# Optimization experiments

Hardware: AMD Instinct MI355X
Metric: run time of the kernel (lower is better)

The kernel has to match this reference:

```python
import jax, jax.numpy as jnp
import numpy as np

B, MAXN, D, H, S = 64, 512, 512, 8, 32
DH = D // H          # per-head dim = 64
N = B * MAXN         # 32768 total nodes
E = 524288           # ~avg degree 16
EPS = 1e-5


def setup_inputs() -> dict:
    key = jax.random.key(0)
    ks = jax.random.split(key, 18)
    s = 0.05
    x_dense = jax.random.normal(ks[0], (B, MAXN, D), jnp.float32)
    x = jax.random.normal(ks[1], (N, D), jnp.float32)
    src = jax.random.randint(ks[2], (E,), 0, N)
    # destinations kept within the same graph as the source
    dst = (src // MAXN) * MAXN + jax.random.randint(ks[3], (E,), 0, MAXN)
    edge_index = jnp.stack([src, dst]).astype(jnp.int32)
    batch = (jnp.arange(N) // MAXN).astype(jnp.int32)  # sorted, 512 nodes/graph
    seed = jax.random.normal(ks[4], (S, 1, D), jnp.float32) * s
    # per-head GCN conv weights concatenated along output dim: [D, H*DH] == [D, D]
    Wk = jax.random.normal(ks[5], (D, D), jnp.float32) * s
    bk = jnp.zeros((D,), jnp.float32)
    Wv = jax.random.normal(ks[6], (D, D), jnp.float32) * s
    bv = jnp.zeros((D,), jnp.float32)
    q_proj_weight = jax.random.normal(ks[7], (D, D), jnp.float32) * s
    Wo = jax.random.normal(ks[8], (D, D), jnp.float32) * s
    bo = jnp.zeros((D,), jnp.float32)
    Wff = jax.random.normal(ks[9], (D, D), jnp.float32) * s
    bff = jnp.zeros((D,), jnp.float32)
    gamma_h = jnp.ones((D,), jnp.float32)
    beta_h = jnp.zeros((D,), jnp.float32)
    gamma_z = jnp.ones((D,), jnp.float32)
    beta_z = jnp.zeros((D,), jnp.float32)
    return dict(x_dense=x_dense, x=x, edge_index=edge_index, batch=batch,
                seed=seed, Wk=Wk, bk=bk, Wv=Wv, bv=bv,
                q_proj_weight=q_proj_weight, Wo=Wo, bo=bo, Wff=Wff, bff=bff,
                gamma_h=gamma_h, beta_h=beta_h, gamma_z=gamma_z, beta_z=beta_z)


def _gcn(x, W, b, src, dst):
    # PyG GCNConv with self-loops + symmetric norm; all H heads fused via W [D, H*DH]
    xw = x @ W                                   # [N, D]
    idx = jnp.arange(N)
    src_f = jnp.concatenate([src, idx])
    dst_f = jnp.concatenate([dst, idx])
    deg = jax.ops.segment_sum(jnp.ones_like(dst_f, dtype=x.dtype), dst_f, num_segments=N)
    dinv = jax.lax.rsqrt(deg)                    # deg >= 1 (self-loops)
    norm = dinv[src_f] * dinv[dst_f]             # [E+N]
    out = jax.ops.segment_sum(xw[src_f] * norm[:, None], dst_f, num_segments=N)
    return out + b


def _to_dense(feat, batch):
    # to_dense_batch for sorted batch vector; padded slots are zeros
    counts = jax.ops.segment_sum(jnp.ones((N,), jnp.int32), batch, num_segments=B)
    start = jnp.cumsum(counts) - counts
    pos = jnp.arange(N) - start[batch]
    return jnp.zeros((B, MAXN, feat.shape[-1]), feat.dtype).at[batch, pos].set(feat)


def _layernorm(x, g, b):
    m = jnp.mean(x, -1, keepdims=True)
    v = jnp.mean(jnp.square(x - m), -1, keepdims=True)
    return (x - m) * jax.lax.rsqrt(v + EPS) * g + b


def reference(x_dense, x, edge_index, batch, seed, Wk, bk, Wv, bv,
              q_proj_weight, Wo, bo, Wff, bff, gamma_h, beta_h, gamma_z, beta_z):
    src, dst = edge_index[0], edge_index[1]
    k_nodes = _gcn(x, Wk, bk, src, dst)          # [N, D] (H heads concat)
    v_nodes = _gcn(x, Wv, bv, src, dst)
    k_dense = _to_dense(k_nodes, batch)          # [B, MAXN, D]
    v_dense = _to_dense(v_nodes, batch)

    # query: seed [S,1,D] repeated over batch -> [S,B,D]; q projection (F.linear)
    query = jnp.broadcast_to(seed, (S, B, D))
    q = jnp.einsum('sbd,ed->sbe', query, q_proj_weight)
    scale = 1.0 / jnp.sqrt(jnp.float32(DH))
    qh = (q * scale).reshape(S, B, H, DH).transpose(1, 2, 0, 3)     # [B,H,S,DH]
    kh = k_dense.reshape(B, MAXN, H, DH).transpose(0, 2, 1, 3)      # [B,H,N,DH]
    vh = v_dense.reshape(B, MAXN, H, DH).transpose(0, 2, 1, 3)
    scores = jnp.einsum('bhsd,bhnd->bhsn', qh, kh)                  # [B,H,S,MAXN]
    attn = jax.nn.softmax(scores, axis=-1)                          # no padding mask (faithful)
    ctx = jnp.einsum('bhsn,bhnd->bhsd', attn, vh)                   # [B,H,S,DH]
    ctx = ctx.transpose(0, 2, 1, 3).reshape(B, S, D)                # heads concat
    attn_out = ctx @ Wo.T + bo                                      # [B,S,D]

    query_bse = jnp.broadcast_to(seed.transpose(1, 0, 2), (B, S, D))
    embed = _layernorm(query_bse + attn_out, gamma_h, beta_h)
    embed = _layernorm(embed + embed @ Wff.T + bff, gamma_z, beta_z)
    return embed
```

## Files before the change

### kernel.cpp

```cpp
#include <hip/hip_runtime.h>
#include <hip/hip_bf16.h>

#define BN   64
#define MAXN 512
#define DIM  512
#define NH   8
#define NS   32
#define NN   32768
#define NE   524288
#define NBLK 256
#define EPB  (NE / NBLK)
#define MP   (2048 * 512)

typedef __hip_bfloat16 bf16;
using bf16x8 = __attribute__((ext_vector_type(8))) short;
using f32x4  = __attribute__((ext_vector_type(4))) float;

__device__ int            g_cnt[NN];
__device__ int            g_off[NN + 1];
__device__ int            g_csr[NE];
__device__ unsigned short g_hist[(long)NBLK * NN];
__device__ unsigned short g_bpfx[(long)NBLK * NN];
__device__ float g_dinv[NN];
__device__ bf16  g_xb[NN * DIM];
__device__ bf16  g_agg[NN * DIM];
__device__ bf16  g_aggT[NN * DIM];
__device__ bf16  g_qf[256 * DIM];
__device__ bf16  g_wob[DIM * DIM];
__device__ bf16  g_wvb[DIM * DIM];
__device__ bf16  g_wvo[DIM * 8 * DIM];
__device__ float g_bvo[DIM];
__device__ bf16  g_wffT[DIM * DIM];
__device__ float g_q[NS * DIM];
__device__ bf16  g_sc[BN * 256 * MAXN];
__device__ bf16  g_cp[BN * NS * 8 * DIM];
__device__ float g_part[4 * MP];
__device__ float g_h1[BN * NS * DIM];
__device__ bf16  g_h1b[BN * NS * DIM];

__device__ inline float bf2f(unsigned short u) {
    union { unsigned int i; float f; } x; x.i = ((unsigned int)u) << 16; return x.f;
}

__device__ inline void gll16(const bf16* g, bf16* l) {
    __builtin_amdgcn_global_load_lds(
        (const __attribute__((address_space(1))) void*)g,
        (__attribute__((address_space(3))) void*)l, 16, 0, 0);
}

__global__ __launch_bounds__(512) void k_hist(const int* __restrict__ dst) {
    __shared__ unsigned int h[NN];
    int p = blockIdx.x, tid = threadIdx.x;
    for (int i = tid; i < NN; i += 512) h[i] = 0;
    __syncthreads();
#pragma unroll
    for (int j = 0; j < EPB / 512; j++) {
        int e = p * EPB + j * 512 + tid;
        atomicAdd(&h[dst[e]], 1u);
    }
    __syncthreads();
    unsigned short* out = g_hist + (long)p * NN;
    for (int i = tid; i < NN; i += 512) out[i] = (unsigned short)h[i];
}

__global__ __launch_bounds__(256) void k_colscan() {
    int v = blockIdx.x * 256 + threadIdx.x;
    unsigned int s = 0;
#pragma unroll 8
    for (int p = 0; p < NBLK; p++) {
        unsigned int hh = g_hist[(long)p * NN + v];
        g_bpfx[(long)p * NN + v] = (unsigned short)s;
        s += hh;
    }
    g_cnt[v] = (int)s;
    g_dinv[v] = rsqrtf(1.0f + (float)s);
}

__global__ void k_scan() {
    __shared__ int part[1024];
    int t = threadIdx.x;
    int base = t * 32;
    int loc[32]; int s = 0;
#pragma unroll
    for (int i = 0; i < 32; i++) { loc[i] = g_cnt[base + i]; s += loc[i]; }
    part[t] = s; __syncthreads();
    for (int o = 1; o < 1024; o <<= 1) {
        int v = (t >= o) ? part[t - o] : 0;
        __syncthreads();
        part[t] += v;
        __syncthreads();
    }
    int ex = (t == 0) ? 0 : part[t - 1];
#pragma unroll
    for (int i = 0; i < 32; i++) { g_off[base + i] = ex; ex += loc[i]; }
    if (t == 1023) g_off[NN] = ex;
}

__global__ __launch_bounds__(512) void k_fillsort(const int* __restrict__ src,
                                                  const int* __restrict__ dst) {
    __shared__ unsigned int l[NN];
    int p = blockIdx.x, tid = threadIdx.x;
    const unsigned short* bp = g_bpfx + (long)p * NN;
    for (int i = tid; i < NN; i += 512) l[i] = bp[i];
    __syncthreads();
#pragma unroll
    for (int j = 0; j < EPB / 512; j++) {
        int e = p * EPB + j * 512 + tid;
        int v = dst[e];
        unsigned int r = atomicAdd(&l[v], 1u);
        g_csr[g_off[v] + r] = src[e];
    }
}

__global__ __launch_bounds__(256) void k_prep(const float* __restrict__ seed,
                                              const float* __restrict__ Wq,
                                              const float* __restrict__ Wo,
                                              const float* __restrict__ Wv,
                                              const float* __restrict__ Wff,
                                              const float* __restrict__ bo,
                                              const float* __restrict__ bv) {
    int blk = blockIdx.x;
    if (blk < 64) {
        int i = blk * 256 + threadIdx.x;
        int s = i >> 9, e = i & 511;
        const float* sr = seed + s * DIM;
        const float* wr = Wq + e * DIM;
        float a0 = 0.f, a1 = 0.f;
        for (int d = 0; d < DIM; d += 8) {
            float4 a = *(const float4*)(sr + d);
            float4 b = *(const float4*)(wr + d);
            float4 c = *(const float4*)(sr + d + 4);
            float4 w = *(const float4*)(wr + d + 4);
            a0 += a.x * b.x + a.y * b.y + a.z * b.z + a.w * b.w;
            a1 += c.x * w.x + c.y * w.y + c.z * w.z + c.w * w.w;
        }
        g_q[i] = (a0 + a1) * 0.125f;
    } else if (blk < 448) {
        long t = (long)(blk - 64) * 256 + threadIdx.x;
        const float* src; bf16* dstp; long off;
        if (t < 32768)      { src = Wo;  dstp = g_wob;  off = t; }
        else if (t < 65536) { src = Wv;  dstp = g_wvb;  off = t - 32768; }
        else                { src = Wff; dstp = g_wffT; off = t - 65536; }
        long i = off * 8;
        float4 a = *(const float4*)(src + i);
        float4 b = *(const float4*)(src + i + 4);
        float v[8] = {a.x, a.y, a.z, a.w, b.x, b.y, b.z, b.w};
        bf16x8 o;
#pragma unroll
        for (int j = 0; j < 8; j++) { bf16 q = __float2bfloat16(v[j]); o[j] = *(short*)&q; }
        *(bf16x8*)(dstp + i) = o;
    } else {
        int e = (blk - 448) * 256 + threadIdx.x;
        const float* orow = Wo + (long)e * DIM;
        float a0 = 0.f, a1 = 0.f;
        for (int c = 0; c < DIM; c += 8) {
            float4 a = *(const float4*)(bv + c);
            float4 w = *(const float4*)(orow + c);
            float4 xx = *(const float4*)(bv + c + 4);
            float4 u = *(const float4*)(orow + c + 4);
            a0 += a.x * w.x + a.y * w.y + a.z * w.z + a.w * w.w;
            a1 += xx.x * u.x + xx.y * u.y + xx.z * u.z + xx.w * u.w;
        }
        g_bvo[e] = bo[e] + a0 + a1;
    }
}

__device__ __forceinline__ void gemm128(const bf16* __restrict__ A, long lda,
                                        const bf16* __restrict__ Bt, long ldb,
                                        long row0, long col0, int kbeg, int kend,
                                        bf16 (*As)[128 * 32], bf16 (*Bs)[128 * 32],
                                        f32x4 acc[4][4]) {
    int tid = threadIdx.x;
    int lane = tid & 63, wave = tid >> 6;
    int wr = wave >> 1, wc = wave & 1;
    int fr = lane & 15, fq = lane >> 4;
    int rchunk = (fq ^ ((fr >> 1) & 3)) * 8;
    int u0 = wave * 128 + lane;
    int sr0 = u0 >> 2, sc0 = ((u0 & 3) ^ ((sr0 >> 1) & 3)) * 8;
    int u1 = u0 + 64;
    int sr1 = u1 >> 2, sc1 = ((u1 & 3) ^ ((sr1 >> 1) & 3)) * 8;

    auto stage = [&](int buf, int kt) {
        gll16(A + (row0 + sr0) * lda + kt + sc0, As[buf] + u0 * 8);
        gll16(A + (row0 + sr1) * lda + kt + sc1, As[buf] + u1 * 8);
        gll16(Bt + (col0 + sr0) * ldb + kt + sc0, Bs[buf] + u0 * 8);
        gll16(Bt + (col0 + sr1) * ldb + kt + sc1, Bs[buf] + u1 * 8);
    };

    stage(0, kbeg);
    __syncthreads();
    for (int kt = kbeg; kt < kend; kt += 32) {
        int buf = ((kt - kbeg) >> 5) & 1;
        if (kt + 32 < kend) stage(buf ^ 1, kt + 32);
        bf16x8 af[4], bfv[4];
#pragma unroll
        for (int mi = 0; mi < 4; mi++)
            af[mi] = *(const bf16x8*)(As[buf] + (wr * 64 + mi * 16 + fr) * 32 + rchunk);
#pragma unroll
        for (int ni = 0; ni < 4; ni++)
            bfv[ni] = *(const bf16x8*)(Bs[buf] + (wc * 64 + ni * 16 + fr) * 32 + rchunk);
#pragma unroll
        for (int mi = 0; mi < 4; mi++)
#pragma unroll
            for (int ni = 0; ni < 4; ni++)
                acc[mi][ni] = __builtin_amdgcn_mfma_f32_16x16x32_bf16(af[mi], bfv[ni], acc[mi][ni], 0, 0, 0);
        __syncthreads();
    }
}

#define ACC_INIT                                             \
    f32x4 acc[4][4];                                         \
    _Pragma("unroll")                                        \
    for (int i = 0; i < 4; i++)                              \
        _Pragma("unroll")                                    \
        for (int j = 0; j < 4; j++) acc[i][j] = (f32x4){0.f, 0.f, 0.f, 0.f}; \
    int lane = threadIdx.x & 63, wave = threadIdx.x >> 6;    \
    int wr = wave >> 1, wc = wave & 1;                       \
    int fr = lane & 15, fq = lane >> 4;

__global__ __launch_bounds__(256) void k_xbqf(const float* __restrict__ x,
                                              const float* __restrict__ Wk) {
    __shared__ bf16 As[2][128 * 32];
    __shared__ bf16 Bs[2][128 * 32];
    int blk = blockIdx.x;
    if (blk < 8192) {
        long i = (long)blk * (256 * 8) + (long)threadIdx.x * 8;
        int node = (int)(i >> 9);
        float w = g_dinv[node];
        float4 a = *(const float4*)(x + i);
        float4 b = *(const float4*)(x + i + 4);
        float v[8] = {a.x, a.y, a.z, a.w, b.x, b.y, b.z, b.w};
        bf16x8 o;
#pragma unroll
        for (int j = 0; j < 8; j++) { bf16 t = __float2bfloat16(v[j] * w); o[j] = *(short*)&t; }
        *(bf16x8*)(g_xb + i) = o;
    } else if (blk < 8704) {
        int i = (blk - 8192) * 256 + threadIdx.x;
        int hs = i >> 9, d = i & 511;
        int h = hs >> 5, s = hs & 31;
        const float* qr = g_q + s * DIM + h * 64;
        const float* wr = Wk + d * DIM + h * 64;
        float a0 = 0.f, a1 = 0.f;
        for (int t2 = 0; t2 < 64; t2 += 8) {
            float4 a = *(const float4*)(qr + t2);
            float4 w = *(const float4*)(wr + t2);
            float4 c = *(const float4*)(qr + t2 + 4);
            float4 u = *(const float4*)(wr + t2 + 4);
            a0 += a.x * w.x + a.y * w.y + a.z * w.z + a.w * w.w;
            a1 += c.x * u.x + c.y * u.y + c.z * u.z + c.w * u.w;
        }
        g_qf[i] = __float2bfloat16(a0 + a1);
    } else {
        int wi = blk - 8704;
        int bx = wi & 3, by = (wi >> 2) & 3, h = wi >> 4;
        ACC_INIT
        long row0 = (long)bx * 128, col0 = (long)by * 128;
        gemm128(g_wob, DIM, g_wvb, DIM, row0, col0, h * 64, h * 64 + 64, As, Bs, acc);
#pragma unroll
        for (int mi = 0; mi < 4; mi++)
#pragma unroll
            for (int ni = 0; ni < 4; ni++) {
                long col = col0 + wc * 64 + ni * 16 + fr;
#pragma unroll
                for (int r = 0; r < 4; r++) {
                    long row = row0 + wr * 64 + mi * 16 + fq * 4 + r;
                    g_wvo[row * 4096 + h * 512 + col] = __float2bfloat16(acc[mi][ni][r]);
                }
            }
    }
}

__global__ __launch_bounds__(256) void k_gather() {
    int bid = blockIdx.x;
    int lb = (bid & 7) * 1024 + (bid >> 3);
    int wave = threadIdx.x >> 6, lane = threadIdx.x & 63;
    int node = lb * 4 + wave;

    bf16x8 sv = ((const bf16x8*)(g_xb + (long)node * DIM))[lane];
    float acc[8];
#pragma unroll
    for (int j = 0; j < 8; j++) acc[j] = bf2f((unsigned short)sv[j]);

    int e = g_off[node], e1 = g_off[node + 1];
    for (; e + 8 <= e1; e += 8) {
        bf16x8 r[8];
#pragma unroll
        for (int q = 0; q < 8; q++)
            r[q] = ((const bf16x8*)(g_xb + (long)g_csr[e + q] * DIM))[lane];
#pragma unroll
        for (int j = 0; j < 8; j++) {
            float s01 = bf2f((unsigned short)r[0][j]) + bf2f((unsigned short)r[1][j]);
            float s23 = bf2f((unsigned short)r[2][j]) + bf2f((unsigned short)r[3][j]);
            float s45 = bf2f((unsigned short)r[4][j]) + bf2f((unsigned short)r[5][j]);
            float s67 = bf2f((unsigned short)r[6][j]) + bf2f((unsigned short)r[7][j]);
            acc[j] += (s01 + s23) + (s45 + s67);
        }
    }
    for (; e < e1; e++) {
        bf16x8 r0 = ((const bf16x8*)(g_xb + (long)g_csr[e] * DIM))[lane];
#pragma unroll
        for (int j = 0; j < 8; j++) acc[j] += bf2f((unsigned short)r0[j]);
    }
    float dd = g_dinv[node];
    bf16x8 o;
#pragma unroll
    for (int j = 0; j < 8; j++) { bf16 t = __float2bfloat16(acc[j] * dd); o[j] = *(short*)&t; }
    ((bf16x8*)(g_agg + (long)node * DIM))[lane] = o;
}

__global__ __launch_bounds__(256) void k_aggsc() {
    __shared__ __align__(16) char smem[32768];
    int blk = blockIdx.x;
    if (blk < 512) {
        bf16 (*As)[128 * 32] = (bf16(*)[128 * 32])smem;
        bf16 (*Bs)[128 * 32] = (bf16(*)[128 * 32])(smem + 16384);
        int b = blk & 63, bx = (blk >> 6) & 1, by = blk >> 7;
        ACC_INIT
        long row0 = (long)bx * 128, col0 = (long)by * 128;
        gemm128(g_qf, DIM, g_agg + (long)b * (MAXN * DIM), DIM, row0, col0, 0, DIM, As, Bs, acc);
        bf16* out = g_sc + (long)b * (256 * MAXN);
#pragma unroll
        for (int mi = 0; mi < 4; mi++)
#pragma unroll
            for (int ni = 0; ni < 4; ni++) {
                long col = col0 + wc * 64 + ni * 16 + fr;
#pragma unroll
                for (int r = 0; r < 4; r++) {
                    long row = row0 + wr * 64 + mi * 16 + fq * 4 + r;
                    out[row * MAXN + col] = __float2bfloat16(acc[mi][ni][r]);
                }
            }
    } else {
        unsigned short (*L)[72] = (unsigned short(*)[72])smem;
        int id = blk - 512;
        int b = id >> 6, t = id & 63;
        int n0 = (t & 7) * 64, d0 = (t >> 3) * 64;
        int tid = threadIdx.x;
        const unsigned short* src = (const unsigned short*)g_agg + ((long)b * 512 + n0) * 512 + d0;
#pragma unroll
        for (int p = 0; p < 2; p++) {
            int r = (tid >> 3) + 32 * p, c = (tid & 7) * 8;
            *(int4*)&L[r][c] = *(const int4*)(src + (long)r * 512 + c);
        }
        __syncthreads();
        unsigned short* dst = (unsigned short*)g_aggT + ((long)b * 512 + d0) * 512 + n0;
#pragma unroll
        for (int p = 0; p < 2; p++) {
            int dr = (tid >> 3) + 32 * p, c0 = (tid & 7) * 8;
            unsigned short tmp[8];
#pragma unroll
            for (int j = 0; j < 8; j++) tmp[j] = L[c0 + j][dr];
            *(int4*)(dst + (long)dr * 512 + c0) = *(int4*)tmp;
        }
    }
}

__global__ __launch_bounds__(256) void k_soft() {
    int w = threadIdx.x >> 6, lane = threadIdx.x & 63;
    unsigned short* base = (unsigned short*)g_sc + ((long)blockIdx.x * 16 + w * 4) * MAXN;
#pragma unroll
    for (int r = 0; r < 4; r++) {
        unsigned short* row = base + (long)r * MAXN;
        float v[8]; float m = -1e30f;
#pragma unroll
        for (int k = 0; k < 8; k++) { v[k] = bf2f(row[lane + 64 * k]); m = fmaxf(m, v[k]); }
#pragma unroll
        for (int o = 32; o > 0; o >>= 1) m = fmaxf(m, __shfl_xor(m, o));
        float sum = 0.f;
#pragma unroll
        for (int k = 0; k < 8; k++) { v[k] = __expf(v[k] - m); sum += v[k]; }
#pragma unroll
        for (int o = 32; o > 0; o >>= 1) sum += __shfl_xor(sum, o);
        float inv = 1.0f / sum;
#pragma unroll
        for (int k = 0; k < 8; k++) {
            bf16 t = __float2bfloat16(v[k] * inv);
            row[lane + 64 * k] = *(unsigned short*)&t;
        }
    }
}

__global__ __launch_bounds__(256) void k_pvg() {
    __shared__ bf16 As[2][128 * 32];
    __shared__ bf16 Bs[2][128 * 32];
    int blk = blockIdx.x;
    int b = blk & 63, bx = (blk >> 6) & 1, by = (blk >> 7) & 1, dh = blk >> 8;
    ACC_INIT
    long row0 = (long)bx * 128, col0 = (long)by * 128;
    gemm128(g_sc + (long)b * (256 * MAXN), MAXN,
            g_aggT + (long)b * (DIM * MAXN) + (long)dh * (256 * MAXN), MAXN,
            row0, col0, 0, MAXN, As, Bs, acc);
#pragma unroll
    for (int mi = 0; mi < 4; mi++)
#pragma unroll
        for (int ni = 0; ni < 4; ni++) {
            long col = col0 + wc * 64 + ni * 16 + fr;
#pragma unroll
            for (int r = 0; r < 4; r++) {
                long row = row0 + wr * 64 + mi * 16 + fq * 4 + r;
                g_cp[((long)b * NS + (row & 31)) * 4096 + (row >> 5) * 512 + dh * 256 + col] =
                    __float2bfloat16(acc[mi][ni][r]);
            }
        }
}

__global__ __launch_bounds__(256) void k_vo() {
    __shared__ bf16 As[2][128 * 32];
    __shared__ bf16 Bs[2][128 * 32];
    ACC_INIT
    int z = blockIdx.z;
    long row0 = (long)blockIdx.x * 128, col0 = (long)blockIdx.y * 128;
    gemm128(g_cp, 4096, g_wvo, 4096, row0, col0, z * 1024, z * 1024 + 1024, As, Bs, acc);
    float* out = g_part + (long)z * MP;
#pragma unroll
    for (int mi = 0; mi < 4; mi++)
#pragma unroll
        for (int ni = 0; ni < 4; ni++) {
            long col = col0 + wc * 64 + ni * 16 + fr;
#pragma unroll
            for (int r = 0; r < 4; r++) {
                long row = row0 + wr * 64 + mi * 16 + fq * 4 + r;
                out[row * DIM + col] = acc[mi][ni][r];
            }
        }
}

__global__ __launch_bounds__(256) void k_ffn() {
    __shared__ bf16 As[2][128 * 32];
    __shared__ bf16 Bs[2][128 * 32];
    ACC_INIT
    int z = blockIdx.z;
    long row0 = (long)blockIdx.x * 128, col0 = (long)blockIdx.y * 128;
    gemm128(g_h1b, DIM, g_wffT, DIM, row0, col0, z * 128, z * 128 + 128, As, Bs, acc);
    float* out = g_part + (long)z * MP;
#pragma unroll
    for (int mi = 0; mi < 4; mi++)
#pragma unroll
        for (int ni = 0; ni < 4; ni++) {
            long col = col0 + wc * 64 + ni * 16 + fr;
#pragma unroll
            for (int r = 0; r < 4; r++) {
                long row = row0 + wr * 64 + mi * 16 + fq * 4 + r;
                out[row * DIM + col] = acc[mi][ni][r];
            }
        }
}

__device__ inline float blockReduceSum(float v, float* red, int tid) {
#pragma unroll
    for (int o = 32; o > 0; o >>= 1) v += __shfl_xor(v, o);
    __syncthreads();
    if ((tid & 63) == 0) red[tid >> 6] = v;
    __syncthreads();
    return red[0] + red[1] + red[2] + red[3];
}

__global__ __launch_bounds__(256) void k_ln1(const float* __restrict__ seed,
                                             const float* __restrict__ gamma,
                                             const float* __restrict__ beta) {
    __shared__ float red[4];
    int r = blockIdx.x, t = threadIdx.x;
    int s = r & 31;
    long base = (long)r * DIM;
    float v0 = seed[s * DIM + t] + g_bvo[t];
    float v1 = seed[s * DIM + 256 + t] + g_bvo[256 + t];
#pragma unroll
    for (int z = 0; z < 4; z++) {
        v0 += g_part[(long)z * MP + base + t];
        v1 += g_part[(long)z * MP + base + 256 + t];
    }
    float mean = blockReduceSum(v0 + v1, red, t) * (1.0f / DIM);
    float d0 = v0 - mean, d1 = v1 - mean;
    float var = blockReduceSum(d0 * d0 + d1 * d1, red, t) * (1.0f / DIM);
    float ri = rsqrtf(var + 1e-5f);
    float o0 = d0 * ri * gamma[t] + beta[t];
    float o1 = d1 * ri * gamma[256 + t] + beta[256 + t];
    g_h1[base + t] = o0; g_h1[base + 256 + t] = o1;
    g_h1b[base + t] = __float2bfloat16(o0);
    g_h1b[base + 256 + t] = __float2bfloat16(o1);
}

__global__ __launch_bounds__(256) void k_ln2(const float* __restrict__ gamma,
                                             const float* __restrict__ beta,
                                             const float* __restrict__ bff,
                                             float* __restrict__ out) {
    __shared__ float red[4];
    int r = blockIdx.x, t = threadIdx.x;
    long base = (long)r * DIM;
    float v0 = g_h1[base + t] + bff[t];
    float v1 = g_h1[base + 256 + t] + bff[256 + t];
#pragma unroll
    for (int z = 0; z < 4; z++) {
        v0 += g_part[(long)z * MP + base + t];
        v1 += g_part[(long)z * MP + base + 256 + t];
    }
    float mean = blockReduceSum(v0 + v1, red, t) * (1.0f / DIM);
    float d0 = v0 - mean, d1 = v1 - mean;
    float var = blockReduceSum(d0 * d0 + d1 * d1, red, t) * (1.0f / DIM);
    float ri = rsqrtf(var + 1e-5f);
    out[base + t] = d0 * ri * gamma[t] + beta[t];
    out[base + 256 + t] = d1 * ri * gamma[256 + t] + beta[256 + t];
}

extern "C" void kernel_launch(void* const* d_in, const int* in_sizes, int n_in,
                              void* d_out, int out_size, void* d_ws, size_t ws_size,
                              hipStream_t stream) {
    (void)in_sizes; (void)n_in; (void)out_size; (void)d_ws; (void)ws_size;
    const float* x    = (const float*)d_in[1];
    const int*   ei   = (const int*)d_in[2];
    const int*   esrc = ei;
    const int*   edst = ei + NE;
    const float* seed = (const float*)d_in[4];
    const float* Wk   = (const float*)d_in[5];
    const float* Wv   = (const float*)d_in[7];
    const float* bv   = (const float*)d_in[8];
    const float* Wq   = (const float*)d_in[9];
    const float* Wo   = (const float*)d_in[10];
    const float* bo   = (const float*)d_in[11];
    const float* Wff  = (const float*)d_in[12];
    const float* bff  = (const float*)d_in[13];
    const float* gh   = (const float*)d_in[14];
    const float* bh   = (const float*)d_in[15];
    const float* gz   = (const float*)d_in[16];
    const float* bz   = (const float*)d_in[17];
    float* out = (float*)d_out;

    k_hist    <<<NBLK, 512, 0, stream>>>(edst);
    k_colscan <<<NN / 256, 256, 0, stream>>>();
    k_scan    <<<1, 1024, 0, stream>>>();
    k_prep    <<<450, 256, 0, stream>>>(seed, Wq, Wo, Wv, Wff, bo, bv);
    k_fillsort<<<NBLK, 512, 0, stream>>>(esrc, edst);
    k_xbqf    <<<8832, 256, 0, stream>>>(x, Wk);
    k_gather  <<<NN / 4, 256, 0, stream>>>();
    k_aggsc   <<<512 + BN * 64, 256, 0, stream>>>();
    k_soft    <<<1024, 256, 0, stream>>>();
    k_pvg     <<<512, 256, 0, stream>>>();
    k_vo      <<<dim3(16, 4, 4), 256, 0, stream>>>();
    k_ln1     <<<BN * NS, 256, 0, stream>>>(seed, gh, bh);
    k_ffn     <<<dim3(16, 4, 4), 256, 0, stream>>>();
    k_ln2     <<<BN * NS, 256, 0, stream>>>(gz, bz, bff, out);
}
```

Baseline: 229.4 us.

## Fuse preprocessing kernels and split each node's gather across four waves

```diff
diff --git a/kernel.cpp b/kernel.cpp
--- a/kernel.cpp
+++ b/kernel.cpp
@@ -48,80 +48,29 @@
         (__attribute__((address_space(3))) void*)l, 16, 0, 0);
 }
 
-__global__ __launch_bounds__(512) void k_hist(const int* __restrict__ dst) {
+__global__ __launch_bounds__(512) void k_histprep(const int* __restrict__ dst,
+                                                  const float* __restrict__ seed,
+                                                  const float* __restrict__ Wq,
+                                                  const float* __restrict__ Wo,
+                                                  const float* __restrict__ Wv,
+                                                  const float* __restrict__ Wff,
+                                                  const float* __restrict__ bo,
+                                                  const float* __restrict__ bv) {
     __shared__ unsigned int h[NN];
-    int p = blockIdx.x, tid = threadIdx.x;
-    for (int i = tid; i < NN; i += 512) h[i] = 0;
-    __syncthreads();
-#pragma unroll
-    for (int j = 0; j < EPB / 512; j++) {
-        int e = p * EPB + j * 512 + tid;
-        atomicAdd(&h[dst[e]], 1u);
-    }
-    __syncthreads();
-    unsigned short* out = g_hist + (long)p * NN;
-    for (int i = tid; i < NN; i += 512) out[i] = (unsigned short)h[i];
-}
-
-__global__ __launch_bounds__(256) void k_colscan() {
-    int v = blockIdx.x * 256 + threadIdx.x;
-    unsigned int s = 0;
-#pragma unroll 8
-    for (int p = 0; p < NBLK; p++) {
-        unsigned int hh = g_hist[(long)p * NN + v];
-        g_bpfx[(long)p * NN + v] = (unsigned short)s;
-        s += hh;
-    }
-    g_cnt[v] = (int)s;
-    g_dinv[v] = rsqrtf(1.0f + (float)s);
-}
-
-__global__ void k_scan() {
-    __shared__ int part[1024];
-    int t = threadIdx.x;
-    int base = t * 32;
-    int loc[32]; int s = 0;
-#pragma unroll
-    for (int i = 0; i < 32; i++) { loc[i] = g_cnt[base + i]; s += loc[i]; }
-    part[t] = s; __syncthreads();
-    for (int o = 1; o < 1024; o <<= 1) {
-        int v = (t >= o) ? part[t - o] : 0;
-        __syncthreads();
-        part[t] += v;
-        __syncthreads();
-    }
-    int ex = (t == 0) ? 0 : part[t - 1];
-#pragma unroll
-    for (int i = 0; i < 32; i++) { g_off[base + i] = ex; ex += loc[i]; }
-    if (t == 1023) g_off[NN] = ex;
-}
-
-__global__ __launch_bounds__(512) void k_fillsort(const int* __restrict__ src,
-                                                  const int* __restrict__ dst) {
-    __shared__ unsigned int l[NN];
-    int p = blockIdx.x, tid = threadIdx.x;
-    const unsigned short* bp = g_bpfx + (long)p * NN;
-    for (int i = tid; i < NN; i += 512) l[i] = bp[i];
-    __syncthreads();
-#pragma unroll
-    for (int j = 0; j < EPB / 512; j++) {
-        int e = p * EPB + j * 512 + tid;
-        int v = dst[e];
-        unsigned int r = atomicAdd(&l[v], 1u);
-        g_csr[g_off[v] + r] = src[e];
-    }
-}
-
-__global__ __launch_bounds__(256) void k_prep(const float* __restrict__ seed,
-                                              const float* __restrict__ Wq,
-                                              const float* __restrict__ Wo,
-                                              const float* __restrict__ Wv,
-                                              const float* __restrict__ Wff,
-                                              const float* __restrict__ bo,
-                                              const float* __restrict__ bv) {
-    int blk = blockIdx.x;
-    if (blk < 64) {
-        int i = blk * 256 + threadIdx.x;
+    int blk = blockIdx.x, tid = threadIdx.x;
+    if (blk < NBLK) {
+        for (int i = tid; i < NN; i += 512) h[i] = 0;
+        __syncthreads();
+#pragma unroll
+        for (int j = 0; j < EPB / 512; j++) {
+            int e = blk * EPB + j * 512 + tid;
+            atomicAdd(&h[dst[e]], 1u);
+        }
+        __syncthreads();
+        unsigned short* out = g_hist + (long)blk * NN;
+        for (int i = tid; i < NN; i += 512) out[i] = (unsigned short)h[i];
+    } else if (blk < 288) {
+        int i = (blk - 256) * 512 + tid;
         int s = i >> 9, e = i & 511;
         const float* sr = seed + s * DIM;
         const float* wr = Wq + e * DIM;
@@ -135,8 +84,8 @@
             a1 += c.x * w.x + c.y * w.y + c.z * w.z + c.w * w.w;
         }
         g_q[i] = (a0 + a1) * 0.125f;
-    } else if (blk < 448) {
-        long t = (long)(blk - 64) * 256 + threadIdx.x;
+    } else if (blk < 480) {
+        long t = (long)(blk - 288) * 512 + tid;
         const float* src; bf16* dstp; long off;
         if (t < 32768)      { src = Wo;  dstp = g_wob;  off = t; }
         else if (t < 65536) { src = Wv;  dstp = g_wvb;  off = t - 32768; }
@@ -150,7 +99,7 @@
         for (int j = 0; j < 8; j++) { bf16 q = __float2bfloat16(v[j]); o[j] = *(short*)&q; }
         *(bf16x8*)(dstp + i) = o;
     } else {
-        int e = (blk - 448) * 256 + threadIdx.x;
+        int e = tid;
         const float* orow = Wo + (long)e * DIM;
         float a0 = 0.f, a1 = 0.f;
         for (int c = 0; c < DIM; c += 8) {
@@ -163,6 +112,137 @@
         }
         g_bvo[e] = bo[e] + a0 + a1;
     }
+}
+
+__global__ __launch_bounds__(256) void k_colscan() {
+    int v = blockIdx.x * 256 + threadIdx.x;
+    unsigned int s = 0;
+#pragma unroll 8
+    for (int p = 0; p < NBLK; p++) {
+        unsigned int hh = g_hist[(long)p * NN + v];
+        g_bpfx[(long)p * NN + v] = (unsigned short)s;
+        s += hh;
+    }
+    g_cnt[v] = (int)s;
+    g_dinv[v] = rsqrtf(1.0f + (float)s);
+}
+
+__global__ void k_scan() {
+    __shared__ int part[1024];
+    int t = threadIdx.x;
+    int base = t * 32;
+    int loc[32]; int s = 0;
+#pragma unroll
+    for (int i = 0; i < 32; i++) { loc[i] = g_cnt[base + i]; s += loc[i]; }
+    part[t] = s; __syncthreads();
+    for (int o = 1; o < 1024; o <<= 1) {
+        int v = (t >= o) ? part[t - o] : 0;
+        __syncthreads();
+        part[t] += v;
+        __syncthreads();
+    }
+    int ex = (t == 0) ? 0 : part[t - 1];
+#pragma unroll
+    for (int i = 0; i < 32; i++) { g_off[base + i] = ex; ex += loc[i]; }
+    if (t == 1023) g_off[NN] = ex;
+}
+
+__global__ __launch_bounds__(512) void k_fillxb(const int* __restrict__ src,
+                                                const int* __restrict__ dst,
+                                                const float* __restrict__ x,
+                                                const float* __restrict__ Wk) {
+    __shared__ unsigned int l[NN];
+    int blk = blockIdx.x, tid = threadIdx.x;
+    if (blk < NBLK) {
+        const unsigned short* bp = g_bpfx + (long)blk * NN;
+        for (int i = tid; i < NN; i += 512) l[i] = bp[i];
+        __syncthreads();
+#pragma unroll
+        for (int j = 0; j < EPB / 512; j++) {
+            int e = blk * EPB + j * 512 + tid;
+            int v = dst[e];
+            unsigned int r = atomicAdd(&l[v], 1u);
+            g_csr[g_off[v] + r] = src[e];
+        }
+    } else if (blk < 4352) {
+        long i = (long)(blk - 256) * (512 * 8) + (long)tid * 8;
+        int node = (int)(i >> 9);
+        float w = g_dinv[node];
+        float4 a = *(const float4*)(x + i);
+        float4 b = *(const float4*)(x + i + 4);
+        float v[8] = {a.x, a.y, a.z, a.w, b.x, b.y, b.z, b.w};
+        bf16x8 o;
+#pragma unroll
+        for (int j = 0; j < 8; j++) { bf16 t = __float2bfloat16(v[j] * w); o[j] = *(short*)&t; }
+        *(bf16x8*)(g_xb + i) = o;
+    } else {
+        int i = (blk - 4352) * 512 + tid;
+        int hs = i >> 9, d = i & 511;
+        int h = hs >> 5, s = hs & 31;
+        const float* qr = g_q + s * DIM + h * 64;
+        const float* wr = Wk + d * DIM + h * 64;
+        float a0 = 0.f, a1 = 0.f;
+        for (int t2 = 0; t2 < 64; t2 += 8) {
+            float4 a = *(const float4*)(qr + t2);
+            float4 w = *(const float4*)(wr + t2);
+            float4 c = *(const float4*)(qr + t2 + 4);
+            float4 u = *(const float4*)(wr + t2 + 4);
+            a0 += a.x * w.x + a.y * w.y + a.z * w.z + a.w * w.w;
+            a1 += c.x * u.x + c.y * u.y + c.z * u.z + c.w * u.w;
+        }
+        g_qf[i] = __float2bfloat16(a0 + a1);
+    }
+}
+
+__global__ __launch_bounds__(256) void k_gather2() {
+    __shared__ float sA[4][576];
+    int bid = blockIdx.x;
+    int node = (bid & 7) * 4096 + (bid >> 3);
+    int w = threadIdx.x >> 6, lane = threadIdx.x & 63;
+
+    float2 acc[4];
+#pragma unroll
+    for (int j = 0; j < 4; j++) acc[j] = make_float2(0.f, 0.f);
+
+    auto addrow = [&](int s) {
+        int4 d = ((const int4*)(g_xb + (long)s * DIM))[lane];
+        union { int i; float f; } lo, hi;
+#pragma unroll
+        for (int j = 0; j < 4; j++) {
+            int dw = (j == 0) ? d.x : (j == 1) ? d.y : (j == 2) ? d.z : d.w;
+            lo.i = dw << 16;
+            hi.i = dw & 0xffff0000;
+            acc[j] += make_float2(lo.f, hi.f);
+        }
+    };
+
+    if (w == 0) addrow(node);
+    int e0 = g_off[node], e1 = g_off[node + 1];
+    int deg = e1 - e0;
+    int m16 = e0 + ((deg >> 4) << 4);
+    for (int eb = e0 + w * 4; eb < m16; eb += 16) {
+        int s0 = g_csr[eb], s1 = g_csr[eb + 1], s2 = g_csr[eb + 2], s3 = g_csr[eb + 3];
+        addrow(s0); addrow(s1); addrow(s2); addrow(s3);
+    }
+    for (int e = m16 + w; e < e1; e += 4) addrow(g_csr[e]);
+
+#pragma unroll
+    for (int j = 0; j < 4; j++) {
+        sA[w][lane * 9 + j * 2]     = acc[j].x;
+        sA[w][lane * 9 + j * 2 + 1] = acc[j].y;
+    }
+    __syncthreads();
+
+    int t = threadIdx.x;
+    int idx = (t >> 2) * 9 + 2 * (t & 3);
+    float s0 = 0.f, s1 = 0.f;
+#pragma unroll
+    for (int ww = 0; ww < 4; ww++) { s0 += sA[ww][idx]; s1 += sA[ww][idx + 1]; }
+    float dd = g_dinv[node];
+    bf16 b0 = __float2bfloat16(s0 * dd), b1 = __float2bfloat16(s1 * dd);
+    unsigned int word = (unsigned int)*(unsigned short*)&b0 |
+                        ((unsigned int)*(unsigned short*)&b1 << 16);
+    ((unsigned int*)(g_agg + (long)node * DIM))[t] = word;
 }
 
 __device__ __forceinline__ void gemm128(const bf16* __restrict__ A, long lda,
@@ -218,96 +298,6 @@
     int wr = wave >> 1, wc = wave & 1;                       \
     int fr = lane & 15, fq = lane >> 4;
 
-__global__ __launch_bounds__(256) void k_xbqf(const float* __restrict__ x,
-                                              const float* __restrict__ Wk) {
-    __shared__ bf16 As[2][128 * 32];
-    __shared__ bf16 Bs[2][128 * 32];
-    int blk = blockIdx.x;
-    if (blk < 8192) {
-        long i = (long)blk * (256 * 8) + (long)threadIdx.x * 8;
-        int node = (int)(i >> 9);
-        float w = g_dinv[node];
-        float4 a = *(const float4*)(x + i);
-        float4 b = *(const float4*)(x + i + 4);
-        float v[8] = {a.x, a.y, a.z, a.w, b.x, b.y, b.z, b.w};
-        bf16x8 o;
-#pragma unroll
-        for (int j = 0; j < 8; j++) { bf16 t = __float2bfloat16(v[j] * w); o[j] = *(short*)&t; }
-        *(bf16x8*)(g_xb + i) = o;
-    } else if (blk < 8704) {
-        int i = (blk - 8192) * 256 + threadIdx.x;
-        int hs = i >> 9, d = i & 511;
-        int h = hs >> 5, s = hs & 31;
-        const float* qr = g_q + s * DIM + h * 64;
-        const float* wr = Wk + d * DIM + h * 64;
-        float a0 = 0.f, a1 = 0.f;
-        for (int t2 = 0; t2 < 64; t2 += 8) {
-            float4 a = *(const float4*)(qr + t2);
-            float4 w = *(const float4*)(wr + t2);
-            float4 c = *(const float4*)(qr + t2 + 4);
-            float4 u = *(const float4*)(wr + t2 + 4);
-            a0 += a.x * w.x + a.y * w.y + a.z * w.z + a.w * w.w;
-            a1 += c.x * u.x + c.y * u.y + c.z * u.z + c.w * u.w;
-        }
-        g_qf[i] = __float2bfloat16(a0 + a1);
-    } else {
-        int wi = blk - 8704;
-        int bx = wi & 3, by = (wi >> 2) & 3, h = wi >> 4;
-        ACC_INIT
-        long row0 = (long)bx * 128, col0 = (long)by * 128;
-        gemm128(g_wob, DIM, g_wvb, DIM, row0, col0, h * 64, h * 64 + 64, As, Bs, acc);
-#pragma unroll
-        for (int mi = 0; mi < 4; mi++)
-#pragma unroll
-            for (int ni = 0; ni < 4; ni++) {
-                long col = col0 + wc * 64 + ni * 16 + fr;
-#pragma unroll
-                for (int r = 0; r < 4; r++) {
-                    long row = row0 + wr * 64 + mi * 16 + fq * 4 + r;
-                    g_wvo[row * 4096 + h * 512 + col] = __float2bfloat16(acc[mi][ni][r]);
-                }
-            }
-    }
-}
-
-__global__ __launch_bounds__(256) void k_gather() {
-    int bid = blockIdx.x;
-    int lb = (bid & 7) * 1024 + (bid >> 3);
-    int wave = threadIdx.x >> 6, lane = threadIdx.x & 63;
-    int node = lb * 4 + wave;
-
-    bf16x8 sv = ((const bf16x8*)(g_xb + (long)node * DIM))[lane];
-    float acc[8];
-#pragma unroll
-    for (int j = 0; j < 8; j++) acc[j] = bf2f((unsigned short)sv[j]);
-
-    int e = g_off[node], e1 = g_off[node + 1];
-    for (; e + 8 <= e1; e += 8) {
-        bf16x8 r[8];
-#pragma unroll
-        for (int q = 0; q < 8; q++)
-            r[q] = ((const bf16x8*)(g_xb + (long)g_csr[e + q] * DIM))[lane];
-#pragma unroll
-        for (int j = 0; j < 8; j++) {
-            float s01 = bf2f((unsigned short)r[0][j]) + bf2f((unsigned short)r[1][j]);
-            float s23 = bf2f((unsigned short)r[2][j]) + bf2f((unsigned short)r[3][j]);
-            float s45 = bf2f((unsigned short)r[4][j]) + bf2f((unsigned short)r[5][j]);
-            float s67 = bf2f((unsigned short)r[6][j]) + bf2f((unsigned short)r[7][j]);
-            acc[j] += (s01 + s23) + (s45 + s67);
-        }
-    }
-    for (; e < e1; e++) {
-        bf16x8 r0 = ((const bf16x8*)(g_xb + (long)g_csr[e] * DIM))[lane];
-#pragma unroll
-        for (int j = 0; j < 8; j++) acc[j] += bf2f((unsigned short)r0[j]);
-    }
-    float dd = g_dinv[node];
-    bf16x8 o;
-#pragma unroll
-    for (int j = 0; j < 8; j++) { bf16 t = __float2bfloat16(acc[j] * dd); o[j] = *(short*)&t; }
-    ((bf16x8*)(g_agg + (long)node * DIM))[lane] = o;
-}
-
 __global__ __launch_bounds__(256) void k_aggsc() {
     __shared__ __align__(16) char smem[32768];
     int blk = blockIdx.x;
@@ -330,7 +320,7 @@
                     out[row * MAXN + col] = __float2bfloat16(acc[mi][ni][r]);
                 }
             }
-    } else {
+    } else if (blk < 4608) {
         unsigned short (*L)[72] = (unsigned short(*)[72])smem;
         int id = blk - 512;
         int b = id >> 6, t = id & 63;
@@ -352,6 +342,25 @@
             for (int j = 0; j < 8; j++) tmp[j] = L[c0 + j][dr];
             *(int4*)(dst + (long)dr * 512 + c0) = *(int4*)tmp;
         }
+    } else {
+        bf16 (*As)[128 * 32] = (bf16(*)[128 * 32])smem;
+        bf16 (*Bs)[128 * 32] = (bf16(*)[128 * 32])(smem + 16384);
+        int wi = blk - 4608;
+        int bx = wi & 3, by = (wi >> 2) & 3, h = wi >> 4;
+        ACC_INIT
+        long row0 = (long)bx * 128, col0 = (long)by * 128;
+        gemm128(g_wob, DIM, g_wvb, DIM, row0, col0, h * 64, h * 64 + 64, As, Bs, acc);
+#pragma unroll
+        for (int mi = 0; mi < 4; mi++)
+#pragma unroll
+            for (int ni = 0; ni < 4; ni++) {
+                long col = col0 + wc * 64 + ni * 16 + fr;
+#pragma unroll
+                for (int r = 0; r < 4; r++) {
+                    long row = row0 + wr * 64 + mi * 16 + fq * 4 + r;
+                    g_wvo[row * 4096 + h * 512 + col] = __float2bfloat16(acc[mi][ni][r]);
+                }
+            }
     }
 }
 
@@ -525,14 +534,12 @@
     const float* bz   = (const float*)d_in[17];
     float* out = (float*)d_out;
 
-    k_hist    <<<NBLK, 512, 0, stream>>>(edst);
+    k_histprep<<<481, 512, 0, stream>>>(edst, seed, Wq, Wo, Wv, Wff, bo, bv);
     k_colscan <<<NN / 256, 256, 0, stream>>>();
     k_scan    <<<1, 1024, 0, stream>>>();
-    k_prep    <<<450, 256, 0, stream>>>(seed, Wq, Wo, Wv, Wff, bo, bv);
-    k_fillsort<<<NBLK, 512, 0, stream>>>(esrc, edst);
-    k_xbqf    <<<8832, 256, 0, stream>>>(x, Wk);
-    k_gather  <<<NN / 4, 256, 0, stream>>>();
-    k_aggsc   <<<512 + BN * 64, 256, 0, stream>>>();
+    k_fillxb  <<<4608, 512, 0, stream>>>(esrc, edst, x, Wk);
+    k_gather2 <<<NN, 256, 0, stream>>>();
+    k_aggsc   <<<4736, 256, 0, stream>>>();
     k_soft    <<<1024, 256, 0, stream>>>();
     k_pvg     <<<512, 256, 0, stream>>>();
     k_vo      <<<dim3(16, 4, 4), 256, 0, stream>>>();
```

After: 243.5 us. 6.2% more time.

## Stage per-graph feature tiles in LDS for neighbor aggregation; pack histogram stores

Applied to the files above, without the earlier changes.

```diff
diff --git a/kernel.cpp b/kernel.cpp
--- a/kernel.cpp
+++ b/kernel.cpp
@@ -51,7 +51,7 @@
 __global__ __launch_bounds__(512) void k_hist(const int* __restrict__ dst) {
     __shared__ unsigned int h[NN];
     int p = blockIdx.x, tid = threadIdx.x;
-    for (int i = tid; i < NN; i += 512) h[i] = 0;
+    for (int i = tid; i < NN / 4; i += 512) ((int4*)h)[i] = make_int4(0, 0, 0, 0);
     __syncthreads();
 #pragma unroll
     for (int j = 0; j < EPB / 512; j++) {
@@ -59,21 +59,26 @@
         atomicAdd(&h[dst[e]], 1u);
     }
     __syncthreads();
-    unsigned short* out = g_hist + (long)p * NN;
-    for (int i = tid; i < NN; i += 512) out[i] = (unsigned short)h[i];
+    unsigned int* out32 = (unsigned int*)(g_hist + (long)p * NN);
+    for (int i = tid; i < NN / 2; i += 512)
+        out32[i] = h[2 * i] | (h[2 * i + 1] << 16);
 }
 
 __global__ __launch_bounds__(256) void k_colscan() {
-    int v = blockIdx.x * 256 + threadIdx.x;
-    unsigned int s = 0;
+    int v2 = blockIdx.x * 256 + threadIdx.x;
+    const unsigned int* H = (const unsigned int*)g_hist;
+    unsigned int* B = (unsigned int*)g_bpfx;
+    unsigned int s0 = 0, s1 = 0;
 #pragma unroll 8
     for (int p = 0; p < NBLK; p++) {
-        unsigned int hh = g_hist[(long)p * NN + v];
-        g_bpfx[(long)p * NN + v] = (unsigned short)s;
-        s += hh;
-    }
-    g_cnt[v] = (int)s;
-    g_dinv[v] = rsqrtf(1.0f + (float)s);
+        unsigned int hh = H[(long)p * (NN / 2) + v2];
+        B[(long)p * (NN / 2) + v2] = s0 | (s1 << 16);
+        s0 += hh & 0xffffu; s1 += hh >> 16;
+    }
+    g_cnt[2 * v2] = (int)s0;
+    g_cnt[2 * v2 + 1] = (int)s1;
+    g_dinv[2 * v2] = rsqrtf(1.0f + (float)s0);
+    g_dinv[2 * v2 + 1] = rsqrtf(1.0f + (float)s1);
 }
 
 __global__ void k_scan() {
@@ -100,8 +105,12 @@
                                                   const int* __restrict__ dst) {
     __shared__ unsigned int l[NN];
     int p = blockIdx.x, tid = threadIdx.x;
-    const unsigned short* bp = g_bpfx + (long)p * NN;
-    for (int i = tid; i < NN; i += 512) l[i] = bp[i];
+    const unsigned int* bp32 = (const unsigned int*)(g_bpfx + (long)p * NN);
+    for (int i = tid; i < NN / 2; i += 512) {
+        unsigned int v = bp32[i];
+        uint2 o = make_uint2(v & 0xffffu, v >> 16);
+        ((uint2*)l)[i] = o;
+    }
     __syncthreads();
 #pragma unroll
     for (int j = 0; j < EPB / 512; j++) {
@@ -137,13 +146,13 @@
         g_q[i] = (a0 + a1) * 0.125f;
     } else if (blk < 448) {
         long t = (long)(blk - 64) * 256 + threadIdx.x;
-        const float* src; bf16* dstp; long off;
-        if (t < 32768)      { src = Wo;  dstp = g_wob;  off = t; }
-        else if (t < 65536) { src = Wv;  dstp = g_wvb;  off = t - 32768; }
-        else                { src = Wff; dstp = g_wffT; off = t - 65536; }
+        const float* srcp; bf16* dstp; long off;
+        if (t < 32768)      { srcp = Wo;  dstp = g_wob;  off = t; }
+        else if (t < 65536) { srcp = Wv;  dstp = g_wvb;  off = t - 32768; }
+        else                { srcp = Wff; dstp = g_wffT; off = t - 65536; }
         long i = off * 8;
-        float4 a = *(const float4*)(src + i);
-        float4 b = *(const float4*)(src + i + 4);
+        float4 a = *(const float4*)(srcp + i);
+        float4 b = *(const float4*)(srcp + i + 4);
         float v[8] = {a.x, a.y, a.z, a.w, b.x, b.y, b.z, b.w};
         bf16x8 o;
 #pragma unroll
@@ -270,42 +279,37 @@
     }
 }
 
-__global__ __launch_bounds__(256) void k_gather() {
-    int bid = blockIdx.x;
-    int lb = (bid & 7) * 1024 + (bid >> 3);
-    int wave = threadIdx.x >> 6, lane = threadIdx.x & 63;
-    int node = lb * 4 + wave;
-
-    bf16x8 sv = ((const bf16x8*)(g_xb + (long)node * DIM))[lane];
-    float acc[8];
-#pragma unroll
-    for (int j = 0; j < 8; j++) acc[j] = bf2f((unsigned short)sv[j]);
-
-    int e = g_off[node], e1 = g_off[node + 1];
-    for (; e + 8 <= e1; e += 8) {
-        bf16x8 r[8];
-#pragma unroll
-        for (int q = 0; q < 8; q++)
-            r[q] = ((const bf16x8*)(g_xb + (long)g_csr[e + q] * DIM))[lane];
-#pragma unroll
-        for (int j = 0; j < 8; j++) {
-            float s01 = bf2f((unsigned short)r[0][j]) + bf2f((unsigned short)r[1][j]);
-            float s23 = bf2f((unsigned short)r[2][j]) + bf2f((unsigned short)r[3][j]);
-            float s45 = bf2f((unsigned short)r[4][j]) + bf2f((unsigned short)r[5][j]);
-            float s67 = bf2f((unsigned short)r[6][j]) + bf2f((unsigned short)r[7][j]);
-            acc[j] += (s01 + s23) + (s45 + s67);
-        }
-    }
-    for (; e < e1; e++) {
-        bf16x8 r0 = ((const bf16x8*)(g_xb + (long)g_csr[e] * DIM))[lane];
-#pragma unroll
-        for (int j = 0; j < 8; j++) acc[j] += bf2f((unsigned short)r0[j]);
-    }
-    float dd = g_dinv[node];
-    bf16x8 o;
-#pragma unroll
-    for (int j = 0; j < 8; j++) { bf16 t = __float2bfloat16(acc[j] * dd); o[j] = *(short*)&t; }
-    ((bf16x8*)(g_agg + (long)node * DIM))[lane] = o;
+__global__ __launch_bounds__(512) void k_spmm() {
+    __shared__ bf16 T[512 * 64];
+    int blk = blockIdx.x;
+    int b = blk & 63, ft = blk >> 6;
+    int tid = threadIdx.x;
+    const bf16* srcp = g_xb + ((long)b * 512) * 512 + ft * 64;
+#pragma unroll
+    for (int c = 0; c < 8; c++) {
+        int u = tid + 512 * c;
+        int row = u >> 3, col = (u & 7) * 8;
+        gll16(srcp + (long)row * 512 + col, T + u * 8);
+    }
+    __syncthreads();
+
+    int w = tid >> 6, lane = tid & 63;
+    const unsigned short* Tl = (const unsigned short*)T;
+    for (int nl = 0; nl < 64; nl++) {
+        int lrow = w * 64 + nl;
+        int node = b * 512 + lrow;
+        float acc = bf2f(Tl[lrow * 64 + lane]);
+        int e = g_off[node], e1 = g_off[node + 1];
+        for (; e + 2 <= e1; e += 2) {
+            int s0 = g_csr[e] & 511, s1 = g_csr[e + 1] & 511;
+            float f0 = bf2f(Tl[s0 * 64 + lane]);
+            float f1 = bf2f(Tl[s1 * 64 + lane]);
+            acc += f0 + f1;
+        }
+        if (e < e1) acc += bf2f(Tl[(g_csr[e] & 511) * 64 + lane]);
+        bf16 q = __float2bfloat16(acc * g_dinv[node]);
+        ((unsigned short*)g_agg)[(long)node * 512 + ft * 64 + lane] = *(unsigned short*)&q;
+    }
 }
 
 __global__ __launch_bounds__(256) void k_aggsc() {
@@ -526,12 +530,12 @@
     float* out = (float*)d_out;
 
     k_hist    <<<NBLK, 512, 0, stream>>>(edst);
-    k_colscan <<<NN / 256, 256, 0, stream>>>();
+    k_colscan <<<NN / 512, 256, 0, stream>>>();
     k_scan    <<<1, 1024, 0, stream>>>();
     k_prep    <<<450, 256, 0, stream>>>(seed, Wq, Wo, Wv, Wff, bo, bv);
     k_fillsort<<<NBLK, 512, 0, stream>>>(esrc, edst);
     k_xbqf    <<<8832, 256, 0, stream>>>(x, Wk);
-    k_gather  <<<NN / 4, 256, 0, stream>>>();
+    k_spmm    <<<512, 512, 0, stream>>>();
     k_aggsc   <<<512 + BN * 64, 256, 0, stream>>>();
     k_soft    <<<1024, 256, 0, stream>>>();
     k_pvg     <<<512, 256, 0, stream>>>();
```

Measured after the change: 313.8 us. 1.37x slower.
